# Performance work log

Hardware: AMD Instinct MI355X
Metric: run time of the kernel (lower is better)

The kernel has to match this reference:

```python
import jax, jax.numpy as jnp
import numpy as np


def setup_inputs() -> dict:
    key = jax.random.key(0)
    k1, k2, k3, k4 = jax.random.split(key, 4)
    B, IN, OUT, S = 8192, 2048, 3072, 8
    scale = 1.0 / (IN ** 0.5)
    x = jax.random.normal(k1, (B, IN), dtype=jnp.float32)
    subject_ids = jax.random.randint(k2, (B,), 0, S, dtype=jnp.int64)
    weights = jax.random.normal(k3, (S, IN, OUT), dtype=jnp.float32) * scale
    bias = jax.random.normal(k4, (S, OUT), dtype=jnp.float32) * scale
    return {"x": x, "subject_ids": subject_ids, "weights": weights, "bias": bias}


def reference(x, subject_ids, weights, bias):
    # Math: out[b] = x[b] @ weights[subject_ids[b]] + bias[subject_ids[b]]
    # Avoid materializing the [B, in, out] gathered weight tensor:
    # contract via a one-hot subject selector instead (same math).
    S = weights.shape[0]
    onehot = jax.nn.one_hot(subject_ids, S, dtype=x.dtype)  # [B, S]
    # [B,d] x [S,d,o] x [B,S] -> [B,o]; intermediate is at most [B,S,o]
    out = jnp.einsum('bd,sdo,bs->bo', x, weights, onehot)
    out = out + bias[subject_ids]  # [B, out]
    return out
```

## Files before the change

kernel.cpp:

```cpp
#include <hip/hip_runtime.h>
#include <hip/hip_bf16.h>
#include <stdint.h>

#define B_ROWS 8192
#define K_DIM  2048
#define N_DIM  3072
#define S_NUM  8

#define BM 256
#define BN 256
#define BK 64
#define NT (K_DIM / BK)
#define MAX_T256 40

#define BMF 128
#define BNF 128
#define BKF 32
#define NKF (K_DIM / BKF)
#define MAX_TILES 72
#define LDA 40
#define LDB 40

typedef __bf16 bf16x8 __attribute__((ext_vector_type(8)));
typedef float  f32x4  __attribute__((ext_vector_type(4)));
typedef unsigned int   u32x4 __attribute__((ext_vector_type(4)));
typedef unsigned short u16x8 __attribute__((ext_vector_type(8)));

#define WS_CNT    0
#define WS_OFFS   256
#define WS_T256S  512
#define WS_T256M  768
#define WS_TILES  1024
#define WS_TILEM  1536
#define WS_RANK   4096
#define WS_PERM   36864
#define WS_XPERM  262144
#define WS_WT     34865152
#define WS_NEED   135528448ULL

__device__ __forceinline__ unsigned int f2bf_pk(float lo, float hi) {
#if __has_builtin(__builtin_amdgcn_cvt_pk_bf16_f32)
    typedef __bf16 bf16x2_t __attribute__((ext_vector_type(2)));
    bf16x2_t v = __builtin_amdgcn_cvt_pk_bf16_f32(lo, hi);
    return __builtin_bit_cast(unsigned int, v);
#else
    unsigned int a = __builtin_bit_cast(unsigned int, lo);
    unsigned int b = __builtin_bit_cast(unsigned int, hi);
    a += 0x7FFFu + ((a >> 16) & 1u);
    b += 0x7FFFu + ((b >> 16) & 1u);
    return (a >> 16) | (b & 0xFFFF0000u);
#endif
}

__device__ __forceinline__ void gl_lds16(const void* g, void* l) {
    __builtin_amdgcn_global_load_lds(
        (const __attribute__((address_space(1))) void*)g,
        (__attribute__((address_space(3))) void*)l, 16, 0, 0);
}

__global__ __launch_bounds__(1024)
void prep_kernel(const int* __restrict__ ids,
                 int* __restrict__ cnt, int* __restrict__ offs,
                 int* __restrict__ t256s, int* __restrict__ t256m,
                 int* __restrict__ tfs, int* __restrict__ tfm,
                 unsigned short* __restrict__ perm, int* __restrict__ rank) {
    __shared__ int lcnt[S_NUM];
    const int tid = threadIdx.x;
    if (tid < S_NUM) lcnt[tid] = 0;
    __syncthreads();
    const int lane = tid & 63;
    #pragma unroll
    for (int c = 0; c < B_ROWS / 1024; ++c) {
        const int b = c * 1024 + tid;
        const int s = ids[b];
        #pragma unroll
        for (int sub = 0; sub < S_NUM; ++sub) {
            unsigned long long m = __ballot(s == sub);
            if (s == sub) {
                int prefix = __popcll(m & ((1ull << lane) - 1ull));
                int leader = __ffsll((unsigned long long)m) - 1;
                int base = 0;
                if (lane == leader) base = atomicAdd(&lcnt[sub], __popcll(m));
                base = __shfl(base, leader);
                perm[sub * B_ROWS + base + prefix] = (unsigned short)b;
                rank[b] = base + prefix;
            }
        }
    }
    __syncthreads();
    if (tid == 0) {
        int t = 0, tf = 0, o = 0;
        for (int s2 = 0; s2 < S_NUM; ++s2) {
            const int c2 = lcnt[s2];
            cnt[s2] = c2; offs[s2] = o; o += c2;
            for (int m0 = 0; m0 < c2; m0 += BM)  { t256s[t] = s2; t256m[t] = m0; ++t; }
            for (int m0 = 0; m0 < c2; m0 += BMF) { tfs[tf] = s2;  tfm[tf] = m0;  ++tf; }
        }
        for (; t < MAX_T256; ++t)    { t256s[t] = -1; t256m[t] = 0; }
        for (; tf < MAX_TILES; ++tf) { tfs[tf]  = -1; tfm[tf]  = 0; }
    }
}

__global__ void convert_x_kernel(const float* __restrict__ x,
                                 const int* __restrict__ ids,
                                 const int* __restrict__ rank,
                                 const int* __restrict__ offs,
                                 unsigned short* __restrict__ xq) {
    const int b = blockIdx.x;
    const int dst = offs[ids[b]] + rank[b];
    const float* src = x + (size_t)b * K_DIM + threadIdx.x * 8;
    f32x4 v0 = *(const f32x4*)(src + 0);
    f32x4 v1 = *(const f32x4*)(src + 4);
    u32x4 p = { f2bf_pk(v0[0], v0[1]), f2bf_pk(v0[2], v0[3]),
                f2bf_pk(v1[0], v1[1]), f2bf_pk(v1[2], v1[3]) };
    *(u32x4*)(xq + (size_t)dst * K_DIM + threadIdx.x * 8) = p;
}

__global__ __launch_bounds__(256)
void convert_w_kernel(const float* __restrict__ w,
                      unsigned short* __restrict__ wt) {
    const int kt = blockIdx.x;
    const int nt = blockIdx.y;
    const int s  = blockIdx.z;
    __shared__ __align__(16) unsigned short lds[128 * 64];

    const int tid = threadIdx.x;
    {
        const int nseg  = tid & 7;
        const int rbase = tid >> 3;
        #pragma unroll
        for (int i = 0; i < 4; ++i) {
            const int r = i * 32 + rbase;
            const float* src = w + ((size_t)s * K_DIM + kt * 128 + r) * N_DIM
                                 + nt * 64 + nseg * 8;
            f32x4 v0 = *(const f32x4*)(src + 0);
            f32x4 v1 = *(const f32x4*)(src + 4);
            u32x4 p = { f2bf_pk(v0[0], v0[1]), f2bf_pk(v0[2], v0[3]),
                        f2bf_pk(v1[0], v1[1]), f2bf_pk(v1[2], v1[3]) };
            const int g = nseg ^ ((r >> 3) & 7);
            *(u32x4*)&lds[r * 64 + g * 8] = p;
        }
    }
    __syncthreads();
    {
        const int kseg  = tid & 15;
        const int nbase = tid >> 4;
        #pragma unroll
        for (int j = 0; j < 4; ++j) {
            const int n = j * 16 + nbase;
            u16x8 o;
            #pragma unroll
            for (int m = 0; m < 8; ++m) {
                const int r = kseg * 8 + m;
                const int g = (n >> 3) ^ ((r >> 3) & 7);
                o[m] = lds[r * 64 + g * 8 + (n & 7)];
            }
            unsigned short* dst = wt + ((size_t)s * N_DIM + nt * 64 + n) * K_DIM
                                     + kt * 128 + kseg * 8;
            *(u16x8*)dst = o;
        }
    }
}

__global__ __launch_bounds__(512, 2)
void gemm256_kernel(const unsigned short* __restrict__ xq,
                    const unsigned short* __restrict__ wt,
                    const float* __restrict__ bias,
                    const int* __restrict__ cnt,
                    const int* __restrict__ offs,
                    const int* __restrict__ tile_s,
                    const int* __restrict__ tile_m,
                    const unsigned short* __restrict__ perm,
                    float* __restrict__ out) {
    const int s = tile_s[blockIdx.x];
    if (s < 0) return;
    const int row0 = tile_m[blockIdx.x];
    const int rows = min(BM, cnt[s] - row0);
    const int n0   = blockIdx.y * BN;

    __shared__ __align__(16) char smem[131072 + 1024];
    int* prow = (int*)(smem + 131072);

    const int tid = threadIdx.x;
    if (tid < BM) {
        int rr = (tid < rows) ? tid : (rows - 1);
        prow[tid] = (int)perm[s * B_ROWS + row0 + rr];
    }

    const int lane = tid & 63;
    const int w    = tid >> 6;
    const int wr   = w >> 2;
    const int wc   = w & 3;
    const int l15  = lane & 15;
    const int quad = lane >> 4;

    const int srow  = w * 8 + (lane >> 3);
    const int sperm = ((lane & 7) ^ (lane >> 3)) << 3;
    const int rowA0 = offs[s] + row0;
    const unsigned short* aSrc = xq + (size_t)(rowA0 + srow) * K_DIM + sperm;
    const unsigned short* bSrc = wt + ((size_t)s * N_DIM + n0 + srow) * K_DIM + sperm;
    char* const aDst = smem + w * 1024;
    char* const bDst = smem + 65536 + w * 1024;

    auto stageA = [&](int half, int tt, int bb) {
        int ttc = (tt < NT) ? tt : (NT - 1);
        const unsigned short* g = aSrc + (size_t)half * (128 * K_DIM) + ttc * BK;
        char* d = aDst + (bb * 2 + half) * 16384;
        gl_lds16(g, d);
        gl_lds16(g + 64 * K_DIM, d + 8192);
    };
    auto stageB = [&](int half, int tt, int bb) {
        int ttc = (tt < NT) ? tt : (NT - 1);
        const unsigned short* g = bSrc + (size_t)half * (128 * K_DIM) + ttc * BK;
        char* d = bDst + (bb * 2 + half) * 16384;
        gl_lds16(g, d);
        gl_lds16(g + 64 * K_DIM, d + 8192);
    };

    bf16x8 af[4][2], bf0[2][2], bf1[2][2];
    auto ldsA = [&](int mh, int bb) {
        const char* base = smem + (bb * 2 + wr) * 16384;
        #pragma unroll
        for (int mt = 0; mt < 4; ++mt) {
            const int row = mh * 64 + mt * 16 + l15;
            #pragma unroll
            for (int kk = 0; kk < 2; ++kk) {
                const int kb = ((kk * 4 + quad) ^ (l15 & 7)) << 4;
                af[mt][kk] = *(const bf16x8*)(base + row * 128 + kb);
            }
        }
    };
    auto ldsB = [&](int nh, int bb, bf16x8 (*dst)[2]) {
        const char* base = smem + 65536 + (bb * 2 + (wc >> 1)) * 16384;
        #pragma unroll
        for (int nt = 0; nt < 2; ++nt) {
            const int row = (wc & 1) * 64 + nh * 32 + nt * 16 + l15;
            #pragma unroll
            for (int kk = 0; kk < 2; ++kk) {
                const int kb = ((kk * 4 + quad) ^ (l15 & 7)) << 4;
                dst[nt][kk] = *(const bf16x8*)(base + row * 128 + kb);
            }
        }
    };

    f32x4 acc[8][4] = {};
    auto mmac = [&](bf16x8 (*b)[2], int mh, int nh) {
        #pragma unroll
        for (int kk = 0; kk < 2; ++kk)
            #pragma unroll
            for (int mt = 0; mt < 4; ++mt)
                #pragma unroll
                for (int nt = 0; nt < 2; ++nt)
                    acc[mh * 4 + mt][nh * 2 + nt] =
                        __builtin_amdgcn_mfma_f32_16x16x32_bf16(
                            af[mt][kk], b[nt][kk],
                            acc[mh * 4 + mt][nh * 2 + nt], 0, 0, 0);
    };

    stageA(0, 0, 0); stageA(1, 0, 0);
    stageB(0, 0, 0); stageB(1, 0, 0);
    stageB(0, 1, 1);
    asm volatile("s_waitcnt vmcnt(2)" ::: "memory");
    __builtin_amdgcn_s_barrier();

    for (int T = 0; T < NT; ++T) {
        const int bb = T & 1, nb = bb ^ 1;
        ldsA(0, bb); ldsB(0, bb, bf0);
        stageB(1, T + 1, nb);
        __builtin_amdgcn_s_barrier();
        __builtin_amdgcn_s_setprio(1);
        mmac(bf0, 0, 0);
        __builtin_amdgcn_s_setprio(0);
        __builtin_amdgcn_s_barrier();
        ldsB(1, bb, bf1);
        stageA(0, T + 1, nb);
        __builtin_amdgcn_s_barrier();
        __builtin_amdgcn_s_setprio(1);
        mmac(bf1, 0, 1);
        __builtin_amdgcn_s_setprio(0);
        __builtin_amdgcn_s_barrier();
        ldsA(1, bb);
        stageA(1, T + 1, nb);
        __builtin_amdgcn_s_barrier();
        __builtin_amdgcn_s_setprio(1);
        mmac(bf1, 1, 1);
        __builtin_amdgcn_s_setprio(0);
        __builtin_amdgcn_s_barrier();
        stageB(0, T + 2, bb);
        asm volatile("s_waitcnt vmcnt(2)" ::: "memory");
        __builtin_amdgcn_s_barrier();
        __builtin_amdgcn_s_setprio(1);
        mmac(bf0, 1, 0);
        __builtin_amdgcn_s_setprio(0);
        __builtin_amdgcn_s_barrier();
    }

    asm volatile("s_waitcnt vmcnt(0)" ::: "memory");

    float bvals[4];
    #pragma unroll
    for (int nt = 0; nt < 4; ++nt)
        bvals[nt] = bias[s * N_DIM + n0 + wc * 64 + nt * 16 + l15];

    #pragma unroll
    for (int mt = 0; mt < 8; ++mt) {
        #pragma unroll
        for (int r = 0; r < 4; ++r) {
            const int rl = wr * 128 + mt * 16 + quad * 4 + r;
            if (rl < rows) {
                float* op = out + (size_t)prow[rl] * N_DIM + n0 + wc * 64 + l15;
                #pragma unroll
                for (int nt = 0; nt < 4; ++nt)
                    op[nt * 16] = acc[mt][nt][r] + bvals[nt];
            }
        }
    }
}

__global__ __launch_bounds__(256, 3)
void subject_gemm_fb(const float* __restrict__ x,
                     const float* __restrict__ w,
                     const float* __restrict__ bias,
                     const int* __restrict__ cnt,
                     const int* __restrict__ tile_s,
                     const int* __restrict__ tile_m,
                     const unsigned short* __restrict__ perm,
                     float* __restrict__ out) {
    const int s = tile_s[blockIdx.x];
    if (s < 0) return;
    const int row0 = tile_m[blockIdx.x];
    const int rows = min(BMF, cnt[s] - row0);
    const int n0   = blockIdx.y * BNF;

    __shared__ __align__(16) unsigned short sA[BMF * LDA];
    __shared__ __align__(16) unsigned short sB[BNF * LDB];
    __shared__ int prow[BMF];

    const int tid = threadIdx.x;
    if (tid < BMF) {
        int rr = (tid < rows) ? tid : (rows - 1);
        prow[tid] = (int)perm[s * B_ROWS + row0 + rr];
    }
    __syncthreads();

    const int ar = tid >> 1;
    const int ah = tid & 1;
    const float* xp = x + (size_t)prow[ar] * K_DIM + ah * 16;
    const int bn  = tid & 127;
    const int bk2 = tid >> 7;
    const float* wp = w + (size_t)s * ((size_t)K_DIM * N_DIM)
                        + (size_t)(bk2 * 16) * N_DIM + (n0 + bn);

    const int lane = tid & 63;
    const int wid  = tid >> 6;
    const int wm   = (wid >> 1) * 64;
    const int wn   = (wid & 1) * 64;
    const int l15  = lane & 15;
    const int quad = lane >> 4;

    f32x4 acc[4][4] = {};
    f32x4 a0, a1, a2, a3;
    float bv[16];
    {
        a0 = *(const f32x4*)(xp + 0);  a1 = *(const f32x4*)(xp + 4);
        a2 = *(const f32x4*)(xp + 8);  a3 = *(const f32x4*)(xp + 12);
        #pragma unroll
        for (int i = 0; i < 16; ++i) bv[i] = wp[(size_t)i * N_DIM];
    }

    for (int ks = 0; ks < NKF; ++ks) {
        u32x4 pa0 = { f2bf_pk(a0[0],a0[1]), f2bf_pk(a0[2],a0[3]),
                      f2bf_pk(a1[0],a1[1]), f2bf_pk(a1[2],a1[3]) };
        u32x4 pa1 = { f2bf_pk(a2[0],a2[1]), f2bf_pk(a2[2],a2[3]),
                      f2bf_pk(a3[0],a3[1]), f2bf_pk(a3[2],a3[3]) };
        u32x4 pb0 = { f2bf_pk(bv[0],bv[1]),   f2bf_pk(bv[2],bv[3]),
                      f2bf_pk(bv[4],bv[5]),   f2bf_pk(bv[6],bv[7]) };
        u32x4 pb1 = { f2bf_pk(bv[8],bv[9]),   f2bf_pk(bv[10],bv[11]),
                      f2bf_pk(bv[12],bv[13]), f2bf_pk(bv[14],bv[15]) };

        __syncthreads();
        *(u32x4*)&sA[ar * LDA + ah * 16 + 0] = pa0;
        *(u32x4*)&sA[ar * LDA + ah * 16 + 8] = pa1;
        *(u32x4*)&sB[bn * LDB + bk2 * 16 + 0] = pb0;
        *(u32x4*)&sB[bn * LDB + bk2 * 16 + 8] = pb1;
        __syncthreads();

        if (ks + 1 < NKF) {
            const float* xq2 = xp + (ks + 1) * BKF;
            a0 = *(const f32x4*)(xq2 + 0);  a1 = *(const f32x4*)(xq2 + 4);
            a2 = *(const f32x4*)(xq2 + 8);  a3 = *(const f32x4*)(xq2 + 12);
            const float* wq = wp + (size_t)((ks + 1) * BKF) * N_DIM;
            #pragma unroll
            for (int i = 0; i < 16; ++i) bv[i] = wq[(size_t)i * N_DIM];
        }

        bf16x8 af[4], bfr[4];
        #pragma unroll
        for (int mt = 0; mt < 4; ++mt)
            af[mt] = *(const bf16x8*)&sA[(wm + mt * 16 + l15) * LDA + quad * 8];
        #pragma unroll
        for (int nt = 0; nt < 4; ++nt)
            bfr[nt] = *(const bf16x8*)&sB[(wn + nt * 16 + l15) * LDB + quad * 8];

        #pragma unroll
        for (int mt = 0; mt < 4; ++mt)
            #pragma unroll
            for (int nt = 0; nt < 4; ++nt)
                acc[mt][nt] = __builtin_amdgcn_mfma_f32_16x16x32_bf16(
                    af[mt], bfr[nt], acc[mt][nt], 0, 0, 0);
    }

    float bvals[4];
    #pragma unroll
    for (int nt = 0; nt < 4; ++nt)
        bvals[nt] = bias[s * N_DIM + n0 + wn + nt * 16 + l15];
    #pragma unroll
    for (int mt = 0; mt < 4; ++mt) {
        #pragma unroll
        for (int r = 0; r < 4; ++r) {
            int rl = wm + mt * 16 + quad * 4 + r;
            if (rl < rows) {
                float* op = out + (size_t)prow[rl] * N_DIM + n0 + wn + l15;
                #pragma unroll
                for (int nt = 0; nt < 4; ++nt)
                    op[nt * 16] = acc[mt][nt][r] + bvals[nt];
            }
        }
    }
}

extern "C" void kernel_launch(void* const* d_in, const int* in_sizes, int n_in,
                              void* d_out, int out_size, void* d_ws, size_t ws_size,
                              hipStream_t stream) {
    const float* x    = (const float*)d_in[0];
    const int*   sid  = (const int*)d_in[1];
    const float* w    = (const float*)d_in[2];
    const float* bias = (const float*)d_in[3];
    float* out = (float*)d_out;

    char* ws = (char*)d_ws;
    int* cnt    = (int*)(ws + WS_CNT);
    int* offs   = (int*)(ws + WS_OFFS);
    int* t256s  = (int*)(ws + WS_T256S);
    int* t256m  = (int*)(ws + WS_T256M);
    int* tfs    = (int*)(ws + WS_TILES);
    int* tfm    = (int*)(ws + WS_TILEM);
    int* rank   = (int*)(ws + WS_RANK);
    unsigned short* perm = (unsigned short*)(ws + WS_PERM);

    hipLaunchKernelGGL(prep_kernel, dim3(1), dim3(1024), 0, stream,
                       sid, cnt, offs, t256s, t256m, tfs, tfm, perm, rank);

    if (ws_size >= WS_NEED) {
        unsigned short* xq = (unsigned short*)(ws + WS_XPERM);
        unsigned short* wt = (unsigned short*)(ws + WS_WT);
        hipLaunchKernelGGL(convert_x_kernel, dim3(B_ROWS), dim3(256), 0, stream,
                           x, sid, rank, offs, xq);
        hipLaunchKernelGGL(convert_w_kernel, dim3(K_DIM / 128, N_DIM / 64, S_NUM),
                           dim3(256), 0, stream, w, wt);
        dim3 grid(MAX_T256, N_DIM / BN);
        hipLaunchKernelGGL(gemm256_kernel, grid, dim3(512), 0, stream,
                           xq, wt, bias, cnt, offs, t256s, t256m, perm, out);
    } else {
        dim3 grid(MAX_TILES, N_DIM / BNF);
        hipLaunchKernelGGL(subject_gemm_fb, grid, dim3(256), 0, stream,
                           x, w, bias, cnt, tfs, tfm, perm, out);
    }
}
```

Baseline: 506.5 us.

## Unroll K loop by two and deepen global-to-LDS prefetch schedule

Restructures the main GEMM K loop to process two tiles per iteration with fixed buffer indices. Global loads for A and B halves are issued further ahead, up to two tiles, and vmcnt waits are relaxed, with sched_barrier added so the compiler keeps the order. The aim is to hide more global memory latency behind MFMA phases. The price is more complex buffer-hazard reasoning and a risk of LDS overwrite races if any stage lands in a buffer still being read.

```diff
diff --git a/kernel.cpp b/kernel.cpp
--- a/kernel.cpp
+++ b/kernel.cpp
@@ -257,43 +257,50 @@
                             acc[mh * 4 + mt][nh * 2 + nt], 0, 0, 0);
     };
 
-    stageA(0, 0, 0); stageA(1, 0, 0);
-    stageB(0, 0, 0); stageB(1, 0, 0);
-    stageB(0, 1, 1);
-    asm volatile("s_waitcnt vmcnt(2)" ::: "memory");
+    #define VMW(N)                                          \
+        asm volatile("s_waitcnt vmcnt(" #N ")" ::: "memory"); \
+        __builtin_amdgcn_sched_barrier(0);
+    #define PH_BAR1_MMAC_BAR2(B, MH, NH)                \
+        __builtin_amdgcn_s_barrier();                   \
+        __builtin_amdgcn_s_setprio(1);                  \
+        mmac(B, MH, NH);                                \
+        __builtin_amdgcn_s_setprio(0);                  \
+        __builtin_amdgcn_s_barrier();
+
+    stageA(0, 0, 0); stageB(0, 0, 0); stageB(1, 0, 0); stageA(1, 0, 0);
+    stageB(0, 1, 1); stageB(1, 1, 1); stageA(0, 1, 1);
+    VMW(6)
     __builtin_amdgcn_s_barrier();
 
-    for (int T = 0; T < NT; ++T) {
-        const int bb = T & 1, nb = bb ^ 1;
-        ldsA(0, bb); ldsB(0, bb, bf0);
-        stageB(1, T + 1, nb);
-        __builtin_amdgcn_s_barrier();
-        __builtin_amdgcn_s_setprio(1);
-        mmac(bf0, 0, 0);
-        __builtin_amdgcn_s_setprio(0);
-        __builtin_amdgcn_s_barrier();
-        ldsB(1, bb, bf1);
-        stageA(0, T + 1, nb);
-        __builtin_amdgcn_s_barrier();
-        __builtin_amdgcn_s_setprio(1);
-        mmac(bf1, 0, 1);
-        __builtin_amdgcn_s_setprio(0);
-        __builtin_amdgcn_s_barrier();
-        ldsA(1, bb);
-        stageA(1, T + 1, nb);
-        __builtin_amdgcn_s_barrier();
-        __builtin_amdgcn_s_setprio(1);
-        mmac(bf1, 1, 1);
-        __builtin_amdgcn_s_setprio(0);
-        __builtin_amdgcn_s_barrier();
-        stageB(0, T + 2, bb);
-        asm volatile("s_waitcnt vmcnt(2)" ::: "memory");
-        __builtin_amdgcn_s_barrier();
-        __builtin_amdgcn_s_setprio(1);
-        mmac(bf0, 1, 0);
-        __builtin_amdgcn_s_setprio(0);
-        __builtin_amdgcn_s_barrier();
-    }
+    for (int i = 0; i < NT / 2; ++i) {
+        const int E = 2 * i, O = 2 * i + 1;
+        ldsA(0, 0); ldsB(0, 0, bf0);
+        stageA(1, O, 1);
+        PH_BAR1_MMAC_BAR2(bf0, 0, 0)
+        ldsB(1, 0, bf1);
+        PH_BAR1_MMAC_BAR2(bf1, 0, 1)
+        ldsA(1, 0);
+        stageB(0, E + 2, 0);
+        PH_BAR1_MMAC_BAR2(bf1, 1, 1)
+        stageB(1, E + 2, 0);
+        VMW(4)
+        PH_BAR1_MMAC_BAR2(bf0, 1, 0)
+        ldsA(0, 1); ldsB(0, 1, bf0);
+        stageA(0, E + 2, 0);
+        PH_BAR1_MMAC_BAR2(bf0, 0, 0)
+        ldsB(1, 1, bf1);
+        stageA(1, E + 2, 0);
+        PH_BAR1_MMAC_BAR2(bf1, 0, 1)
+        ldsA(1, 1);
+        stageB(0, O + 2, 1);
+        PH_BAR1_MMAC_BAR2(bf1, 1, 1)
+        stageB(1, O + 2, 1);
+        stageA(0, O + 2, 1);
+        VMW(6)
+        PH_BAR1_MMAC_BAR2(bf0, 1, 0)
+    }
+    #undef PH_BAR1_MMAC_BAR2
+    #undef VMW
 
     asm volatile("s_waitcnt vmcnt(0)" ::: "memory");
 
```

Result: faster. 494.7 us (-2.3%).
